# Kernel optimization log

Measured on AMD Instinct MI355X. Metric: run time of the kernel, lower is better.

The kernel has to match this reference:

```python
import jax, jax.numpy as jnp
import numpy as np

NUM_HEADS = 16
WINDOW = 256


def setup_inputs() -> dict:
    key = jax.random.key(0)
    ks = jax.random.split(key, 9)
    B, S, H = 2, 2048, 1024
    sc = 0.02
    return {
        "hidden_states": jax.random.normal(ks[0], (B, S, H), jnp.float32),
        "wq": jax.random.normal(ks[1], (H, H), jnp.float32) * sc,
        "bq": jax.random.normal(ks[2], (H,), jnp.float32) * sc,
        "wk": jax.random.normal(ks[3], (H, H), jnp.float32) * sc,
        "bk": jax.random.normal(ks[4], (H,), jnp.float32) * sc,
        "wv": jax.random.normal(ks[5], (H, H), jnp.float32) * sc,
        "bv": jax.random.normal(ks[6], (H,), jnp.float32) * sc,
        "wo": jax.random.normal(ks[7], (H, H), jnp.float32) * sc,
        "bo": jax.random.normal(ks[8], (H,), jnp.float32) * sc,
    }


def reference(hidden_states, wq, bq, wk, bk, wv, bv, wo, bo):
    B, S, H = hidden_states.shape
    nH, hd = NUM_HEADS, H // NUM_HEADS
    scale = 1.0 / np.sqrt(hd).astype(np.float32)

    def heads(x):  # [B,S,H] -> [B,nH,S,hd]
        return x.reshape(B, S, nH, hd).transpose(0, 2, 1, 3)

    q = heads(hidden_states @ wq.T + bq)
    k = heads(hidden_states @ wk.T + bk)
    v = heads(hidden_states @ wv.T + bv)

    scores = jnp.einsum("bhqd,bhkd->bhqk", q, k) * scale  # [B,nH,S,S]

    # allowed keys for query i: j in [i - WINDOW, i] (causal window)
    i = jnp.arange(S)[:, None]
    j = jnp.arange(S)[None, :]
    allowed = (j <= i) & (j >= i - WINDOW)  # [S,S]

    scores = jnp.where(allowed[None, None], scores, -jnp.inf)
    # original clamps AFTER masking -> -inf becomes -10000 (soft mask)
    scores = jnp.clip(scores, -10000.0, 10000.0)

    probs = jax.nn.softmax(scores, axis=-1)
    probs = jnp.nan_to_num(probs, nan=0.0, posinf=0.0, neginf=0.0)

    out = jnp.einsum("bhqk,bhkd->bhqd", probs, v)  # [B,nH,S,hd]
    out = out.transpose(0, 2, 1, 3).reshape(B, S, H)
    return out @ wo.T + bo
```

## Files before the change

kernel.cpp:

```cpp
#include <hip/hip_runtime.h>
#include <hip/hip_bf16.h>
#include <stdint.h>

typedef __attribute__((ext_vector_type(8))) short short8;
typedef __attribute__((ext_vector_type(4))) float f32x4;
typedef __attribute__((ext_vector_type(4))) unsigned short u16x4;

__device__ __forceinline__ float bf2f(unsigned short u) {
  union { unsigned int u; float f; } x; x.u = ((unsigned int)u) << 16; return x.f;
}
__device__ __forceinline__ unsigned short f2bf(float f) {
  union { float f; unsigned int u; } x; x.f = f;
  unsigned int u = x.u;
  return (unsigned short)((u + 0x7fffu + ((u >> 16) & 1u)) >> 16);
}

__device__ __forceinline__ void gload_lds16(const void* g, void* l) {
  __builtin_amdgcn_global_load_lds(
      (const __attribute__((address_space(1))) void*)g,
      (__attribute__((address_space(3))) void*)l, 16, 0, 0);
}

__global__ void cvt_all(const float* __restrict__ X,
                        const float* __restrict__ w0, const float* __restrict__ w1,
                        const float* __restrict__ w2, const float* __restrict__ w3,
                        unsigned short* __restrict__ Xb,
                        unsigned short* __restrict__ Wb) {
  if (blockIdx.y == 0) {
    int i = (blockIdx.x * 256 + threadIdx.x) * 4;
    f32x4 f = *(const f32x4*)(X + i);
    u16x4 o = { f2bf(f[0]), f2bf(f[1]), f2bf(f[2]), f2bf(f[3]) };
    *(u16x4*)(Xb + i) = o;
  } else {
    int wi = blockIdx.x >> 10;
    const float* s = wi == 0 ? w0 : wi == 1 ? w1 : wi == 2 ? w2 : w3;
    int j = ((blockIdx.x & 1023) * 256 + threadIdx.x) * 4;
    f32x4 f = *(const f32x4*)(s + j);
    u16x4 o = { f2bf(f[0]), f2bf(f[1]), f2bf(f[2]), f2bf(f[3]) };
    *(u16x4*)(Wb + ((size_t)wi << 20) + j) = o;
  }
}

__global__ __launch_bounds__(512, 2)
void gemm_qkv_fused(const unsigned short* __restrict__ A,
                    const unsigned short* __restrict__ Wbase,
                    const float* __restrict__ bq, const float* __restrict__ bk,
                    const float* __restrict__ bv,
                    unsigned short* __restrict__ obf) {
  const int K = 1024, NT = 32;
  constexpr int ASZ = 128 * 32;
  constexpr int BSZ = 3 * 128 * 32;
  __shared__ unsigned short lds[3 * (ASZ + BSZ)];

  int flat = blockIdx.y * 8 + blockIdx.x;
  int swz = (flat & 7) * 32 + (flat >> 3);
  const int n0 = (swz & 7) * 128, m0 = (swz >> 3) * 128;

  const int tid = threadIdx.x, lane = tid & 63, w = tid >> 6;
  const int wr = w >> 1, wc = w & 1;
  const int fr = lane & 15, g = lane >> 4;

  f32x4 acc[3][2][4] = {};

#define STAGE(bi, t)                                                            \
  do {                                                                          \
    unsigned short* lb = lds + (bi) * (ASZ + BSZ);                              \
    {                                                                           \
      int s = tid;                                                              \
      int row = s >> 2;                                                         \
      int gc = (s & 3) ^ ((row >> 1) & 3);                                      \
      gload_lds16(A + (size_t)(m0 + row) * K + (t) * 32 + gc * 8, &lb[s * 8]);  \
    }                                                                           \
    _Pragma("unroll") for (int i = 0; i < 3; ++i) {                             \
      int s = i * 512 + tid;                                                    \
      int row = s >> 2;                        \
      int zz = row >> 7, br = row & 127;                                        \
      int gc = (s & 3) ^ ((row >> 1) & 3);                                      \
      gload_lds16(Wbase + ((size_t)zz << 20) + (size_t)(n0 + br) * K +          \
                      (t) * 32 + gc * 8,                                        \
                  &lb[ASZ + s * 8]);                                            \
    }                                                                           \
  } while (0)

#define COMPUTE(bi)                                                             \
  do {                                                                          \
    unsigned short* lb = lds + (bi) * (ASZ + BSZ);                              \
    short8 af[2], bfr[3][4];                                                    \
    _Pragma("unroll") for (int m = 0; m < 2; ++m) {                             \
      int ra = wr * 32 + m * 16 + fr;                                           \
      af[m] = *(const short8*)&lb[ra * 32 + ((g ^ ((ra >> 1) & 3)) * 8)];       \
    }                                                                           \
    _Pragma("unroll") for (int zz = 0; zz < 3; ++zz)                            \
        _Pragma("unroll") for (int n = 0; n < 4; ++n) {                         \
      int rb2 = zz * 128 + wc * 64 + n * 16 + fr;                               \
      bfr[zz][n] =                                                              \
          *(const short8*)&lb[ASZ + rb2 * 32 + ((g ^ ((rb2 >> 1) & 3)) * 8)];   \
    }                                                                           \
    _Pragma("unroll") for (int zz = 0; zz < 3; ++zz)                            \
        _Pragma("unroll") for (int m = 0; m < 2; ++m)                           \
        _Pragma("unroll") for (int n = 0; n < 4; ++n) {                         \
      if (zz < 2)                                                               \
        acc[zz][m][n] = __builtin_amdgcn_mfma_f32_16x16x32_bf16(                \
            bfr[zz][n], af[m], acc[zz][m][n], 0, 0, 0);                         \
      else                                                                      \
        acc[zz][m][n] = __builtin_amdgcn_mfma_f32_16x16x32_bf16(                \
            af[m], bfr[zz][n], acc[zz][m][n], 0, 0, 0);                         \
    }                                                                           \
  } while (0)

  STAGE(0, 0);
  STAGE(1, 1);
  for (int t = 0; t < NT; ++t) {
    if (t < NT - 1)
      asm volatile("s_waitcnt vmcnt(4)" ::: "memory");
    else
      asm volatile("s_waitcnt vmcnt(0)" ::: "memory");
    __builtin_amdgcn_s_barrier();
    __builtin_amdgcn_sched_barrier(0);
    if (t + 2 < NT) STAGE((t + 2) % 3, t + 2);
    __builtin_amdgcn_s_setprio(1);
    COMPUTE(t % 3);
    __builtin_amdgcn_s_setprio(0);
  }
#undef STAGE
#undef COMPUTE

#pragma unroll
  for (int zz = 0; zz < 2; ++zz) {
    const float* bias = zz == 0 ? bq : bk;
#pragma unroll
    for (int m = 0; m < 2; ++m) {
#pragma unroll
      for (int n = 0; n < 4; ++n) {
        int token = m0 + wr * 32 + m * 16 + fr;
        int col0 = n0 + wc * 64 + n * 16 + g * 4;
        f32x4 bvv = *(const f32x4*)&bias[col0];
        u16x4 pk;
#pragma unroll
        for (int i = 0; i < 4; ++i) pk[i] = f2bf(acc[zz][m][n][i] + bvv[i]);
        int hh = col0 >> 6, d0 = col0 & 63;
        int bb = token >> 11, s0 = token & 2047;
        *(u16x4*)&obf[(((size_t)(zz * 32 + bb * 16 + hh)) * 2048 + s0) * 64 + d0] = pk;
      }
    }
  }
#pragma unroll
  for (int m = 0; m < 2; ++m) {
#pragma unroll
    for (int n = 0; n < 4; ++n) {
      int col = n0 + wc * 64 + n * 16 + fr;
      float bias_v = bv[col];
      int row0 = m0 + wr * 32 + m * 16 + g * 4;
      int hh = col >> 6, d = col & 63;
      int bb = row0 >> 11, s0 = row0 & 2047;
      u16x4 pk;
#pragma unroll
      for (int i = 0; i < 4; ++i) pk[i] = f2bf(acc[2][m][n][i] + bias_v);
      *(u16x4*)&obf[(((size_t)(64 + bb * 16 + hh)) * 64 + d) * 2048 + s0] = pk;
    }
  }
}

__global__ __launch_bounds__(256)
void gemm_oproj(const unsigned short* __restrict__ A,
                const unsigned short* __restrict__ W,
                const float* __restrict__ bias, float* __restrict__ of32) {
  const int K = 1024, NT = 32;
  constexpr int BN = 64;
  constexpr int GX = 1024 / BN;
  constexpr int ASZ = 128 * 32, BSZ = BN * 32;
  __shared__ unsigned short lds[3 * (ASZ + BSZ)];

  constexpr int NWG = GX * 32;
  int flat = blockIdx.y * GX + blockIdx.x;
  int swz = (flat & 7) * (NWG / 8) + (flat >> 3);
  const int n0 = (swz % GX) * BN, m0 = (swz / GX) * 128;

  const int tid = threadIdx.x, lane = tid & 63, w = tid >> 6;
  const int fr = lane & 15, g = lane >> 4;

  f32x4 acc[2][4] = {};

#define STAGE(bi, t)                                                            \
  do {                                                                          \
    unsigned short* lb = lds + (bi) * (ASZ + BSZ);                              \
    _Pragma("unroll") for (int i = 0; i < 2; ++i) {                             \
      int s = i * 256 + tid;                                                    \
      int row = s >> 2;                                                         \
      int gc = (s & 3) ^ ((row >> 1) & 3);                                      \
      gload_lds16(A + (size_t)(m0 + row) * K + (t) * 32 + gc * 8, &lb[s * 8]);  \
    }                                                                           \
    {                                                                           \
      int s = tid;                                                              \
      int row = s >> 2;                                                         \
      int gc = (s & 3) ^ ((row >> 1) & 3);                                      \
      gload_lds16(W + (size_t)(n0 + row) * K + (t) * 32 + gc * 8,               \
                  &lb[ASZ + s * 8]);                                            \
    }                                                                           \
  } while (0)

#define COMPUTE(bi)                                                             \
  do {                                                                          \
    unsigned short* lb = lds + (bi) * (ASZ + BSZ);                              \
    short8 af[2], bfr[4];                                                       \
    _Pragma("unroll") for (int m = 0; m < 2; ++m) {                             \
      int ra = w * 32 + m * 16 + fr;                                            \
      af[m] = *(const short8*)&lb[ra * 32 + ((g ^ ((ra >> 1) & 3)) * 8)];       \
    }                                                                           \
    _Pragma("unroll") for (int n = 0; n < 4; ++n) {                             \
      int rb2 = n * 16 + fr;                                                    \
      bfr[n] = *(const short8*)&lb[ASZ + rb2 * 32 + ((g ^ ((rb2 >> 1) & 3)) * 8)]; \
    }                                                                           \
    _Pragma("unroll") for (int m = 0; m < 2; ++m)                               \
        _Pragma("unroll") for (int n = 0; n < 4; ++n)                           \
        acc[m][n] = __builtin_amdgcn_mfma_f32_16x16x32_bf16(bfr[n], af[m],      \
                                                            acc[m][n], 0, 0, 0);\
  } while (0)

  STAGE(0, 0);
  STAGE(1, 1);
  for (int t = 0; t < NT; ++t) {
    if (t < NT - 1)
      asm volatile("s_waitcnt vmcnt(3)" ::: "memory");
    else
      asm volatile("s_waitcnt vmcnt(0)" ::: "memory");
    __builtin_amdgcn_s_barrier();
    __builtin_amdgcn_sched_barrier(0);
    if (t + 2 < NT) STAGE((t + 2) % 3, t + 2);
    __builtin_amdgcn_s_setprio(1);
    COMPUTE(t % 3);
    __builtin_amdgcn_s_setprio(0);
  }
#undef STAGE
#undef COMPUTE

#pragma unroll
  for (int m = 0; m < 2; ++m) {
#pragma unroll
    for (int n = 0; n < 4; ++n) {
      int token = m0 + w * 32 + m * 16 + fr;
      int col0 = n0 + n * 16 + g * 4;
      f32x4 bvv = *(const f32x4*)&bias[col0];
      f32x4 o;
#pragma unroll
      for (int i = 0; i < 4; ++i) o[i] = acc[m][n][i] + bvv[i];
      *(f32x4*)&of32[(size_t)token * 1024 + col0] = o;
    }
  }
}

__global__ __launch_bounds__(256)
void attn_mfma(const unsigned short* __restrict__ QKV, unsigned short* __restrict__ AO) {
  const int S = 2048;
  const int b = blockIdx.z, h = blockIdx.y;
  const int q0 = blockIdx.x * 128;
  const size_t hb = (size_t)(b * 16 + h);
  const unsigned short* Qh = QKV + hb * (S * 64);
  const unsigned short* Kh = QKV + 4194304 + hb * (S * 64);
  const unsigned short* Vt = QKV + 8388608 + hb * (S * 64);

  const int tid = threadIdx.x;
  const int lane = tid & 63, w = tid >> 6;
  const int c = lane & 15, g = lane >> 4;
  const int qw0 = q0 + 32 * w;

  __shared__ unsigned short Plds[4][1024];
  char* Pb = (char*)&Plds[w][0];

  short8 qa[2][2];
#pragma unroll
  for (int mi = 0; mi < 2; ++mi)
#pragma unroll
    for (int cs = 0; cs < 2; ++cs)
      qa[mi][cs] = *(const short8*)(Qh + (size_t)(qw0 + 16 * mi + c) * 64 + 32 * cs + g * 8);

  f32x4 o[2][4] = {};
  float mrow[2][4], lsum[2][4];
#pragma unroll
  for (int mi = 0; mi < 2; ++mi)
#pragma unroll
    for (int r = 0; r < 4; ++r) { mrow[mi][r] = -1e30f; lsum[mi][r] = 0.f; }

  int kt0 = qw0 - 256; if (kt0 < 0) kt0 = 0;
  const int ktlast = qw0;

  short8 kf[2][2], vf[4];
#pragma unroll
  for (int ni = 0; ni < 2; ++ni)
#pragma unroll
    for (int cs = 0; cs < 2; ++cs)
      kf[ni][cs] = *(const short8*)(Kh + (size_t)(kt0 + 16 * ni + c) * 64 + 32 * cs + g * 8);
#pragma unroll
  for (int ni = 0; ni < 4; ++ni)
    vf[ni] = *(const short8*)(Vt + (size_t)(16 * ni + c) * 2048 + kt0 + g * 8);

  for (int kt = kt0; kt <= ktlast; kt += 32) {
    const int ktn = (kt + 32 <= ktlast) ? kt + 32 : kt;
    short8 kfn[2][2], vfn[4];
#pragma unroll
    for (int ni = 0; ni < 2; ++ni)
#pragma unroll
      for (int cs = 0; cs < 2; ++cs)
        kfn[ni][cs] = *(const short8*)(Kh + (size_t)(ktn + 16 * ni + c) * 64 + 32 * cs + g * 8);
#pragma unroll
    for (int ni = 0; ni < 4; ++ni)
      vfn[ni] = *(const short8*)(Vt + (size_t)(16 * ni + c) * 2048 + ktn + g * 8);

    f32x4 sA[2][2] = {};
#pragma unroll
    for (int mi = 0; mi < 2; ++mi)
#pragma unroll
      for (int ni = 0; ni < 2; ++ni)
#pragma unroll
        for (int cs = 0; cs < 2; ++cs)
          sA[mi][ni] = __builtin_amdgcn_mfma_f32_16x16x32_bf16(qa[mi][cs], kf[ni][cs],
                                                               sA[mi][ni], 0, 0, 0);

    float sv[2][2][4];
#pragma unroll
    for (int mi = 0; mi < 2; ++mi)
#pragma unroll
      for (int ni = 0; ni < 2; ++ni)
#pragma unroll
        for (int r = 0; r < 4; ++r) {
          int q = qw0 + 16 * mi + 4 * g + r;
          int k = kt + 16 * ni + c;
          sv[mi][ni][r] = ((unsigned)(q - k) <= 256u) ? sA[mi][ni][r] * 0.125f : -3.0e38f;
        }

#pragma unroll
    for (int mi = 0; mi < 2; ++mi) {
#pragma unroll
      for (int r = 0; r < 4; ++r) {
        float tm = fmaxf(sv[mi][0][r], sv[mi][1][r]);
        tm = fmaxf(tm, __shfl_xor(tm, 1));
        tm = fmaxf(tm, __shfl_xor(tm, 2));
        tm = fmaxf(tm, __shfl_xor(tm, 4));
        tm = fmaxf(tm, __shfl_xor(tm, 8));
        float mnew = fmaxf(mrow[mi][r], tm);
        float sc = __expf(mrow[mi][r] - mnew);
        mrow[mi][r] = mnew;
        float p0 = __expf(sv[mi][0][r] - mnew);
        float p1 = __expf(sv[mi][1][r] - mnew);
        float ps = p0 + p1;
        ps += __shfl_xor(ps, 1);
        ps += __shfl_xor(ps, 2);
        ps += __shfl_xor(ps, 4);
        ps += __shfl_xor(ps, 8);
        lsum[mi][r] = lsum[mi][r] * sc + ps;
#pragma unroll
        for (int ni = 0; ni < 4; ++ni)
          o[mi][ni][r] *= sc;
        int qloc = 16 * mi + 4 * g + r;
        int xr = (qloc & 12) << 2;
        *(unsigned short*)(Pb + ((qloc * 64 + c * 2) ^ xr)) = f2bf(p0);
        *(unsigned short*)(Pb + ((qloc * 64 + 32 + c * 2) ^ xr)) = f2bf(p1);
      }
    }

#pragma unroll
    for (int mi = 0; mi < 2; ++mi) {
      int qloc = 16 * mi + c;
      short8 pa = *(const short8*)(Pb + ((qloc * 64 + g * 16) ^ ((qloc & 12) << 2)));
#pragma unroll
      for (int ni = 0; ni < 4; ++ni)
        o[mi][ni] = __builtin_amdgcn_mfma_f32_16x16x32_bf16(pa, vf[ni], o[mi][ni], 0, 0, 0);
    }

#pragma unroll
    for (int ni = 0; ni < 2; ++ni)
#pragma unroll
      for (int cs = 0; cs < 2; ++cs)
        kf[ni][cs] = kfn[ni][cs];
#pragma unroll
    for (int ni = 0; ni < 4; ++ni)
      vf[ni] = vfn[ni];
  }

#pragma unroll
  for (int mi = 0; mi < 2; ++mi)
#pragma unroll
    for (int r = 0; r < 4; ++r) {
      float inv = 1.f / lsum[mi][r];
      int q = qw0 + 16 * mi + 4 * g + r;
      unsigned short* row = AO + (size_t)(b * 2048 + q) * 1024 + h * 64 + c;
#pragma unroll
      for (int ni = 0; ni < 4; ++ni)
        row[16 * ni] = f2bf(o[mi][ni][r] * inv);
    }
}

extern "C" void kernel_launch(void* const* d_in, const int* in_sizes, int n_in,
                              void* d_out, int out_size, void* d_ws, size_t ws_size,
                              hipStream_t stream) {
  const float* X  = (const float*)d_in[0];
  const float* wq = (const float*)d_in[1];
  const float* bq = (const float*)d_in[2];
  const float* wk = (const float*)d_in[3];
  const float* bk = (const float*)d_in[4];
  const float* wv = (const float*)d_in[5];
  const float* bv = (const float*)d_in[6];
  const float* wo = (const float*)d_in[7];
  const float* bo = (const float*)d_in[8];
  float* out = (float*)d_out;

  unsigned short* Xb  = (unsigned short*)d_ws;
  unsigned short* Wb  = Xb + 4194304;
  unsigned short* QKV = Wb + 4194304;
  unsigned short* AO  = QKV + 12582912;

  cvt_all<<<dim3(4096, 2), dim3(256), 0, stream>>>(X, wq, wk, wv, wo, Xb, Wb);
  gemm_qkv_fused<<<dim3(8, 32), dim3(512), 0, stream>>>(Xb, Wb, bq, bk, bv, QKV);
  attn_mfma<<<dim3(16, 16, 2), dim3(256), 0, stream>>>(QKV, AO);
  gemm_oproj<<<dim3(16, 32, 1), dim3(256), 0, stream>>>(AO, Wb + 3 * 1048576, bo, out);
}
```

Measured before the change: 89.57 us.

## Interleave QKV prefetch with MFMA and retile O-proj with split-K across waves

The QKV GEMM main loop now issues the next-stage global-to-LDS loads piecewise, interleaved between each of the three weight-group MFMA batches, instead of all at once before compute. The output projection GEMM moves to 128x128 tiles with 512 threads, a K-step of 64 and an 8-chunk XOR swizzle. The two 4-wave groups each process half of every K chunk, and their partial sums are combined through LDS before the bias is added and the result stored. This is meant to improve load/compute overlap and per-tile reuse, at the cost of fewer workgroups (256 instead of 512), a reduction pass, and more registers per thread.

```diff
diff --git a/kernel.cpp b/kernel.cpp
--- a/kernel.cpp
+++ b/kernel.cpp
@@ -62,54 +62,154 @@
 
   f32x4 acc[3][2][4] = {};
 
+#define STAGE_A(bi, t)                                                          \
+  do {                                                                          \
+    int s = tid;                                                                \
+    int row = s >> 2;                                                           \
+    int gc = (s & 3) ^ ((row >> 1) & 3);                                        \
+    gload_lds16(A + (size_t)(m0 + row) * K + (t) * 32 + gc * 8,                 \
+                &lds[(bi) * (ASZ + BSZ) + s * 8]);                              \
+  } while (0)
+
+#define STAGE_W(bi, t, i)                                                       \
+  do {                                                                          \
+    int s = (i) * 512 + tid;                                                    \
+    int row = s >> 2;                                                           \
+    int zz = row >> 7, br = row & 127;                                          \
+    int gc = (s & 3) ^ ((row >> 1) & 3);                                        \
+    gload_lds16(Wbase + ((size_t)zz << 20) + (size_t)(n0 + br) * K +            \
+                    (t) * 32 + gc * 8,                                          \
+                &lds[(bi) * (ASZ + BSZ) + ASZ + s * 8]);                        \
+  } while (0)
+
+  STAGE_A(0, 0); STAGE_W(0, 0, 0); STAGE_W(0, 0, 1); STAGE_W(0, 0, 2);
+  STAGE_A(1, 1); STAGE_W(1, 1, 0); STAGE_W(1, 1, 1); STAGE_W(1, 1, 2);
+
+  for (int t = 0; t < NT; ++t) {
+    if (t < NT - 1)
+      asm volatile("s_waitcnt vmcnt(4)" ::: "memory");
+    else
+      asm volatile("s_waitcnt vmcnt(0)" ::: "memory");
+    __builtin_amdgcn_s_barrier();
+    __builtin_amdgcn_sched_barrier(0);
+
+    const int bi = t % 3, bi2 = (t + 2) % 3;
+    const bool pf = (t + 2 < NT);
+    unsigned short* lb = lds + bi * (ASZ + BSZ);
+
+    if (pf) STAGE_A(bi2, t + 2);
+
+    short8 af[2];
+#pragma unroll
+    for (int m = 0; m < 2; ++m) {
+      int ra = wr * 32 + m * 16 + fr;
+      af[m] = *(const short8*)&lb[ra * 32 + ((g ^ ((ra >> 1) & 3)) * 8)];
+    }
+
+#pragma unroll
+    for (int zz = 0; zz < 3; ++zz) {
+      short8 bfr[4];
+#pragma unroll
+      for (int n = 0; n < 4; ++n) {
+        int rb2 = zz * 128 + wc * 64 + n * 16 + fr;
+        bfr[n] = *(const short8*)&lb[ASZ + rb2 * 32 + ((g ^ ((rb2 >> 1) & 3)) * 8)];
+      }
+      if (pf) STAGE_W(bi2, t + 2, zz);
+      __builtin_amdgcn_s_setprio(1);
+#pragma unroll
+      for (int m = 0; m < 2; ++m)
+#pragma unroll
+        for (int n = 0; n < 4; ++n) {
+          if (zz < 2)
+            acc[zz][m][n] = __builtin_amdgcn_mfma_f32_16x16x32_bf16(
+                bfr[n], af[m], acc[zz][m][n], 0, 0, 0);
+          else
+            acc[zz][m][n] = __builtin_amdgcn_mfma_f32_16x16x32_bf16(
+                af[m], bfr[n], acc[zz][m][n], 0, 0, 0);
+        }
+      __builtin_amdgcn_s_setprio(0);
+    }
+  }
+#undef STAGE_A
+#undef STAGE_W
+
+#pragma unroll
+  for (int zz = 0; zz < 2; ++zz) {
+    const float* bias = zz == 0 ? bq : bk;
+#pragma unroll
+    for (int m = 0; m < 2; ++m) {
+#pragma unroll
+      for (int n = 0; n < 4; ++n) {
+        int token = m0 + wr * 32 + m * 16 + fr;
+        int col0 = n0 + wc * 64 + n * 16 + g * 4;
+        f32x4 bvv = *(const f32x4*)&bias[col0];
+        u16x4 pk;
+#pragma unroll
+        for (int i = 0; i < 4; ++i) pk[i] = f2bf(acc[zz][m][n][i] + bvv[i]);
+        int hh = col0 >> 6, d0 = col0 & 63;
+        int bb = token >> 11, s0 = token & 2047;
+        *(u16x4*)&obf[(((size_t)(zz * 32 + bb * 16 + hh)) * 2048 + s0) * 64 + d0] = pk;
+      }
+    }
+  }
+#pragma unroll
+  for (int m = 0; m < 2; ++m) {
+#pragma unroll
+    for (int n = 0; n < 4; ++n) {
+      int col = n0 + wc * 64 + n * 16 + fr;
+      float bias_v = bv[col];
+      int row0 = m0 + wr * 32 + m * 16 + g * 4;
+      int hh = col >> 6, d = col & 63;
+      int bb = row0 >> 11, s0 = row0 & 2047;
+      u16x4 pk;
+#pragma unroll
+      for (int i = 0; i < 4; ++i) pk[i] = f2bf(acc[2][m][n][i] + bias_v);
+      *(u16x4*)&obf[(((size_t)(64 + bb * 16 + hh)) * 64 + d) * 2048 + s0] = pk;
+    }
+  }
+}
+
+__global__ __launch_bounds__(512, 2)
+void gemm_oproj(const unsigned short* __restrict__ A,
+                const unsigned short* __restrict__ W,
+                const float* __restrict__ bias, float* __restrict__ of32) {
+  const int K = 1024, NT = 16;
+  constexpr int ABUF = 128 * 64;
+  constexpr int BUFSZ = 2 * ABUF;
+  __shared__ unsigned short lds[3 * BUFSZ];
+
+  int flat = blockIdx.y * 8 + blockIdx.x;
+  int swz = (flat & 7) * 32 + (flat >> 3);
+  const int n0 = (swz & 7) * 128, m0 = (swz >> 3) * 128;
+
+  const int tid = threadIdx.x, lane = tid & 63, w = tid >> 6;
+  const int kg = w >> 2, wq = w & 3;
+  const int mt = (wq >> 1) * 64, nt = (wq & 1) * 64;
+  const int fr = lane & 15, g = lane >> 4;
+
+  f32x4 acc[4][4] = {};
+
 #define STAGE(bi, t)                                                            \
   do {                                                                          \
-    unsigned short* lb = lds + (bi) * (ASZ + BSZ);                              \
-    {                                                                           \
-      int s = tid;                                                              \
-      int row = s >> 2;                                                         \
-      int gc = (s & 3) ^ ((row >> 1) & 3);                                      \
-      gload_lds16(A + (size_t)(m0 + row) * K + (t) * 32 + gc * 8, &lb[s * 8]);  \
+    unsigned short* lb = lds + (bi) * BUFSZ;                                    \
+    _Pragma("unroll") for (int i = 0; i < 2; ++i) {                             \
+      int c = i * 512 + tid;                                                    \
+      int row = c >> 3;                                                         \
+      int ch = (c & 7) ^ (row & 7);                                             \
+      gload_lds16(A + (size_t)(m0 + row) * K + (t) * 64 + ch * 8, &lb[c * 8]);  \
     }                                                                           \
-    _Pragma("unroll") for (int i = 0; i < 3; ++i) {                             \
-      int s = i * 512 + tid;                                                    \
-      int row = s >> 2;                        \
-      int zz = row >> 7, br = row & 127;                                        \
-      int gc = (s & 3) ^ ((row >> 1) & 3);                                      \
-      gload_lds16(Wbase + ((size_t)zz << 20) + (size_t)(n0 + br) * K +          \
-                      (t) * 32 + gc * 8,                                        \
-                  &lb[ASZ + s * 8]);                                            \
+    _Pragma("unroll") for (int i = 0; i < 2; ++i) {                             \
+      int c = i * 512 + tid;                                                    \
+      int row = c >> 3;                                                         \
+      int ch = (c & 7) ^ (row & 7);                                             \
+      gload_lds16(W + (size_t)(n0 + row) * K + (t) * 64 + ch * 8,               \
+                  &lb[ABUF + c * 8]);                                           \
     }                                                                           \
   } while (0)
 
-#define COMPUTE(bi)                                                             \
-  do {                                                                          \
-    unsigned short* lb = lds + (bi) * (ASZ + BSZ);                              \
-    short8 af[2], bfr[3][4];                                                    \
-    _Pragma("unroll") for (int m = 0; m < 2; ++m) {                             \
-      int ra = wr * 32 + m * 16 + fr;                                           \
-      af[m] = *(const short8*)&lb[ra * 32 + ((g ^ ((ra >> 1) & 3)) * 8)];       \
-    }                                                                           \
-    _Pragma("unroll") for (int zz = 0; zz < 3; ++zz)                            \
-        _Pragma("unroll") for (int n = 0; n < 4; ++n) {                         \
-      int rb2 = zz * 128 + wc * 64 + n * 16 + fr;                               \
-      bfr[zz][n] =                                                              \
-          *(const short8*)&lb[ASZ + rb2 * 32 + ((g ^ ((rb2 >> 1) & 3)) * 8)];   \
-    }                                                                           \
-    _Pragma("unroll") for (int zz = 0; zz < 3; ++zz)                            \
-        _Pragma("unroll") for (int m = 0; m < 2; ++m)                           \
-        _Pragma("unroll") for (int n = 0; n < 4; ++n) {                         \
-      if (zz < 2)                                                               \
-        acc[zz][m][n] = __builtin_amdgcn_mfma_f32_16x16x32_bf16(                \
-            bfr[zz][n], af[m], acc[zz][m][n], 0, 0, 0);                         \
-      else                                                                      \
-        acc[zz][m][n] = __builtin_amdgcn_mfma_f32_16x16x32_bf16(                \
-            af[m], bfr[zz][n], acc[zz][m][n], 0, 0, 0);                         \
-    }                                                                           \
-  } while (0)
-
   STAGE(0, 0);
   STAGE(1, 1);
+  const int kc = kg * 4 + g;
   for (int t = 0; t < NT; ++t) {
     if (t < NT - 1)
       asm volatile("s_waitcnt vmcnt(4)" ::: "memory");
@@ -118,133 +218,54 @@
     __builtin_amdgcn_s_barrier();
     __builtin_amdgcn_sched_barrier(0);
     if (t + 2 < NT) STAGE((t + 2) % 3, t + 2);
+
+    unsigned short* lb = lds + (t % 3) * BUFSZ;
+    short8 af[4], bf[4];
+#pragma unroll
+    for (int m = 0; m < 4; ++m) {
+      int ra = mt + m * 16 + fr;
+      af[m] = *(const short8*)&lb[ra * 64 + ((kc ^ (ra & 7)) * 8)];
+    }
+#pragma unroll
+    for (int n = 0; n < 4; ++n) {
+      int rb = nt + n * 16 + fr;
+      bf[n] = *(const short8*)&lb[ABUF + rb * 64 + ((kc ^ (rb & 7)) * 8)];
+    }
     __builtin_amdgcn_s_setprio(1);
-    COMPUTE(t % 3);
+#pragma unroll
+    for (int m = 0; m < 4; ++m)
+#pragma unroll
+      for (int n = 0; n < 4; ++n)
+        acc[m][n] = __builtin_amdgcn_mfma_f32_16x16x32_bf16(bf[n], af[m],
+                                                            acc[m][n], 0, 0, 0);
     __builtin_amdgcn_s_setprio(0);
   }
 #undef STAGE
-#undef COMPUTE
-
-#pragma unroll
-  for (int zz = 0; zz < 2; ++zz) {
-    const float* bias = zz == 0 ? bq : bk;
-#pragma unroll
-    for (int m = 0; m < 2; ++m) {
+
+  __syncthreads();
+  float* red = (float*)lds;
+  if (kg == 1) {
+#pragma unroll
+    for (int m = 0; m < 4; ++m)
+#pragma unroll
+      for (int n = 0; n < 4; ++n)
+        *(f32x4*)(red + wq * 4096 + (m * 4 + n) * 256 + lane * 4) = acc[m][n];
+  }
+  __syncthreads();
+  if (kg == 0) {
+#pragma unroll
+    for (int m = 0; m < 4; ++m) {
 #pragma unroll
       for (int n = 0; n < 4; ++n) {
-        int token = m0 + wr * 32 + m * 16 + fr;
-        int col0 = n0 + wc * 64 + n * 16 + g * 4;
+        f32x4 other = *(const f32x4*)(red + wq * 4096 + (m * 4 + n) * 256 + lane * 4);
+        int token = m0 + mt + m * 16 + fr;
+        int col0 = n0 + nt + n * 16 + g * 4;
         f32x4 bvv = *(const f32x4*)&bias[col0];
-        u16x4 pk;
-#pragma unroll
-        for (int i = 0; i < 4; ++i) pk[i] = f2bf(acc[zz][m][n][i] + bvv[i]);
-        int hh = col0 >> 6, d0 = col0 & 63;
-        int bb = token >> 11, s0 = token & 2047;
-        *(u16x4*)&obf[(((size_t)(zz * 32 + bb * 16 + hh)) * 2048 + s0) * 64 + d0] = pk;
+        f32x4 o;
+#pragma unroll
+        for (int i = 0; i < 4; ++i) o[i] = acc[m][n][i] + other[i] + bvv[i];
+        *(f32x4*)&of32[(size_t)token * 1024 + col0] = o;
       }
-    }
-  }
-#pragma unroll
-  for (int m = 0; m < 2; ++m) {
-#pragma unroll
-    for (int n = 0; n < 4; ++n) {
-      int col = n0 + wc * 64 + n * 16 + fr;
-      float bias_v = bv[col];
-      int row0 = m0 + wr * 32 + m * 16 + g * 4;
-      int hh = col >> 6, d = col & 63;
-      int bb = row0 >> 11, s0 = row0 & 2047;
-      u16x4 pk;
-#pragma unroll
-      for (int i = 0; i < 4; ++i) pk[i] = f2bf(acc[2][m][n][i] + bias_v);
-      *(u16x4*)&obf[(((size_t)(64 + bb * 16 + hh)) * 64 + d) * 2048 + s0] = pk;
-    }
-  }
-}
-
-__global__ __launch_bounds__(256)
-void gemm_oproj(const unsigned short* __restrict__ A,
-                const unsigned short* __restrict__ W,
-                const float* __restrict__ bias, float* __restrict__ of32) {
-  const int K = 1024, NT = 32;
-  constexpr int BN = 64;
-  constexpr int GX = 1024 / BN;
-  constexpr int ASZ = 128 * 32, BSZ = BN * 32;
-  __shared__ unsigned short lds[3 * (ASZ + BSZ)];
-
-  constexpr int NWG = GX * 32;
-  int flat = blockIdx.y * GX + blockIdx.x;
-  int swz = (flat & 7) * (NWG / 8) + (flat >> 3);
-  const int n0 = (swz % GX) * BN, m0 = (swz / GX) * 128;
-
-  const int tid = threadIdx.x, lane = tid & 63, w = tid >> 6;
-  const int fr = lane & 15, g = lane >> 4;
-
-  f32x4 acc[2][4] = {};
-
-#define STAGE(bi, t)                                                            \
-  do {                                                                          \
-    unsigned short* lb = lds + (bi) * (ASZ + BSZ);                              \
-    _Pragma("unroll") for (int i = 0; i < 2; ++i) {                             \
-      int s = i * 256 + tid;                                                    \
-      int row = s >> 2;                                                         \
-      int gc = (s & 3) ^ ((row >> 1) & 3);                                      \
-      gload_lds16(A + (size_t)(m0 + row) * K + (t) * 32 + gc * 8, &lb[s * 8]);  \
-    }                                                                           \
-    {                                                                           \
-      int s = tid;                                                              \
-      int row = s >> 2;                                                         \
-      int gc = (s & 3) ^ ((row >> 1) & 3);                                      \
-      gload_lds16(W + (size_t)(n0 + row) * K + (t) * 32 + gc * 8,               \
-                  &lb[ASZ + s * 8]);                                            \
-    }                                                                           \
-  } while (0)
-
-#define COMPUTE(bi)                                                             \
-  do {                                                                          \
-    unsigned short* lb = lds + (bi) * (ASZ + BSZ);                              \
-    short8 af[2], bfr[4];                                                       \
-    _Pragma("unroll") for (int m = 0; m < 2; ++m) {                             \
-      int ra = w * 32 + m * 16 + fr;                                            \
-      af[m] = *(const short8*)&lb[ra * 32 + ((g ^ ((ra >> 1) & 3)) * 8)];       \
-    }                                                                           \
-    _Pragma("unroll") for (int n = 0; n < 4; ++n) {                             \
-      int rb2 = n * 16 + fr;                                                    \
-      bfr[n] = *(const short8*)&lb[ASZ + rb2 * 32 + ((g ^ ((rb2 >> 1) & 3)) * 8)]; \
-    }                                                                           \
-    _Pragma("unroll") for (int m = 0; m < 2; ++m)                               \
-        _Pragma("unroll") for (int n = 0; n < 4; ++n)                           \
-        acc[m][n] = __builtin_amdgcn_mfma_f32_16x16x32_bf16(bfr[n], af[m],      \
-                                                            acc[m][n], 0, 0, 0);\
-  } while (0)
-
-  STAGE(0, 0);
-  STAGE(1, 1);
-  for (int t = 0; t < NT; ++t) {
-    if (t < NT - 1)
-      asm volatile("s_waitcnt vmcnt(3)" ::: "memory");
-    else
-      asm volatile("s_waitcnt vmcnt(0)" ::: "memory");
-    __builtin_amdgcn_s_barrier();
-    __builtin_amdgcn_sched_barrier(0);
-    if (t + 2 < NT) STAGE((t + 2) % 3, t + 2);
-    __builtin_amdgcn_s_setprio(1);
-    COMPUTE(t % 3);
-    __builtin_amdgcn_s_setprio(0);
-  }
-#undef STAGE
-#undef COMPUTE
-
-#pragma unroll
-  for (int m = 0; m < 2; ++m) {
-#pragma unroll
-    for (int n = 0; n < 4; ++n) {
-      int token = m0 + w * 32 + m * 16 + fr;
-      int col0 = n0 + n * 16 + g * 4;
-      f32x4 bvv = *(const f32x4*)&bias[col0];
-      f32x4 o;
-#pragma unroll
-      for (int i = 0; i < 4; ++i) o[i] = acc[m][n][i] + bvv[i];
-      *(f32x4*)&of32[(size_t)token * 1024 + col0] = o;
     }
   }
 }
@@ -412,5 +433,5 @@
   cvt_all<<<dim3(4096, 2), dim3(256), 0, stream>>>(X, wq, wk, wv, wo, Xb, Wb);
   gemm_qkv_fused<<<dim3(8, 32), dim3(512), 0, stream>>>(Xb, Wb, bq, bk, bv, QKV);
   attn_mfma<<<dim3(16, 16, 2), dim3(256), 0, stream>>>(QKV, AO);
-  gemm_oproj<<<dim3(16, 32, 1), dim3(256), 0, stream>>>(AO, Wb + 3 * 1048576, bo, out);
-}
+  gemm_oproj<<<dim3(8, 32), dim3(512), 0, stream>>>(AO, Wb + 3 * 1048576, bo, out);
+}
```

After: 86.31 us. -3.6%, faster.
